# Optimization experiments

Measured on AMD Instinct MI355X. Metric: run time of the kernel, lower is better.

Reference implementation:

```python
import jax, jax.numpy as jnp
import numpy as np

EMBED_DIM = 1024
ZDIM = 128
STD = 0.02


def setup_inputs() -> dict:
    key = jax.random.key(0)
    ks = jax.random.split(key, 12)
    T, S, B, E, Z = 2048, 2048, 4, EMBED_DIM, ZDIM
    return {
        "query": jax.random.normal(ks[0], (T, B, E), jnp.float32),
        "key": jax.random.normal(ks[1], (S, B, E), jnp.float32),
        "Wq": jax.random.normal(ks[2], (2 * E + Z, E), jnp.float32) * STD,
        "bq": jnp.zeros((2 * E + Z,), jnp.float32),
        "Wk": jax.random.normal(ks[3], (Z, E), jnp.float32) * STD,
        "bk": jnp.zeros((Z,), jnp.float32),
        "Wv": jax.random.normal(ks[4], (E, E), jnp.float32) * STD,
        "bv": jnp.zeros((E,), jnp.float32),
        "Wh": jax.random.normal(ks[5], (E, E), jnp.float32) * STD,
        "bh": jnp.zeros((E,), jnp.float32),
        "gamma": jax.random.normal(ks[6], (2, Z), jnp.float32) * STD,
        "beta": jnp.zeros((2, Z), jnp.float32),
    }


def reference(query, key, Wq, bq, Wk, bk, Wv, bv, Wh, bh, gamma, beta):
    E, Z = EMBED_DIM, ZDIM
    scaling = Z ** (-0.5)
    # base: [T, B, 2E+Z]
    base = jnp.einsum('tbe,fe->tbf', query, Wq) + bq
    u = jax.nn.sigmoid(base[..., :E])                      # [T,B,E] output gate
    rq = jax.nn.silu(base[..., E:])                        # [T,B,E+Z]
    r = rq[..., :E]                                        # [T,B,E]
    q = rq[..., E:] * gamma[0] + beta[0]                   # [T,B,Z]
    k = jax.nn.silu(jnp.einsum('sbe,ze->sbz', key, Wk) + bk) * gamma[1] + beta[1]  # [S,B,Z]
    v = jax.nn.silu(jnp.einsum('sbe,fe->sbf', key, Wv) + bv)                       # [S,B,E]
    # softmax attention over context dim
    qk = jnp.einsum('tbz,sbz->bts', q * scaling, k)        # [B,T,S]
    attn = jax.nn.softmax(qk, axis=-1)
    h = jnp.einsum('bts,sbf->tbf', attn, v)                # [T,B,E]
    h = jnp.tanh(jnp.einsum('tbe,fe->tbf', h * r, Wh) + bh)
    out = query + u * (h - query)                          # addcmul
    return out
```

## Files before the change

### kernel.cpp

```cpp
#include <hip/hip_runtime.h>
#include <cstdint>
#include <cstddef>

using short8  = __attribute__((ext_vector_type(8))) short;
using floatx4 = __attribute__((ext_vector_type(4))) float;

#define DEV __device__ __forceinline__

DEV float u2f(unsigned short u){
  union { unsigned int i; float f; } c; c.i = ((unsigned int)u) << 16; return c.f;
}
DEV unsigned short f2u(float f){
  union { float f; unsigned int i; } c; c.f = f;
  unsigned int i = c.i;
  i += 0x7fffu + ((i >> 16) & 1u);
  return (unsigned short)(i >> 16);
}
DEV float sigmoidf_(float x){ return 1.0f / (1.0f + __expf(-x)); }
DEV float siluf_(float x){ return x / (1.0f + __expf(-x)); }

#define ASYNC_LD16(g, l) __builtin_amdgcn_global_load_lds( \
    (const __attribute__((address_space(1))) unsigned int*)(g), \
    (__attribute__((address_space(3))) unsigned int*)(l), 16, 0, 0)

#define MFMA_BF16 __builtin_amdgcn_mfma_f32_16x16x32_bf16

#define SBAR() asm volatile("s_barrier" ::: "memory")
#define LGKM0() asm volatile("s_waitcnt lgkmcnt(0)" ::: "memory")

constexpr float SCALING = 0.088388347648318447f;

__global__ __launch_bounds__(256) void cast_act(
    const float* __restrict__ q, const float* __restrict__ k,
    unsigned short* __restrict__ qo, unsigned short* __restrict__ ko)
{
  const int bid = blockIdx.x;
  const int e = threadIdx.x * 4;
  const float* src; unsigned short* dst;
  if (bid < 8192) {
    src = q + (long long)bid * 1024;
    dst = qo + (long long)bid * 1024;
  } else {
    const int m = bid - 8192;
    const int s = m >> 2, b = m & 3;
    src = k + (long long)m * 1024;
    dst = ko + ((long long)b * 2048 + s) * 1024;
  }
  const float4 v = *(const float4*)(src + e);
  ushort4 o; o.x=f2u(v.x); o.y=f2u(v.y); o.z=f2u(v.z); o.w=f2u(v.w);
  *(ushort4*)(dst + e) = o;
}

__global__ __launch_bounds__(256) void cast_w(
    const float* __restrict__ Wq, const float* __restrict__ Wk,
    const float* __restrict__ Wv, const float* __restrict__ Wh,
    unsigned short* __restrict__ oq, unsigned short* __restrict__ ok,
    unsigned short* __restrict__ ov, unsigned short* __restrict__ oh)
{
  const int bid = blockIdx.x;
  const int e = threadIdx.x * 4;
  const float* src; unsigned short* dst;
  if (bid < 2176)      { src = Wq + (long long)bid * 1024;        dst = oq + (long long)bid * 1024; }
  else if (bid < 2304) { src = Wk + (long long)(bid-2176) * 1024; dst = ok + (long long)(bid-2176) * 1024; }
  else if (bid < 3328) { src = Wv + (long long)(bid-2304) * 1024; dst = ov + (long long)(bid-2304) * 1024; }
  else                 { src = Wh + (long long)(bid-3328) * 1024; dst = oh + (long long)(bid-3328) * 1024; }
  const float4 v = *(const float4*)(src + e);
  ushort4 o; o.x=f2u(v.x); o.y=f2u(v.y); o.z=f2u(v.z); o.w=f2u(v.w);
  *(ushort4*)(dst + e) = o;
}

template<int EPI>
__global__ __launch_bounds__(256, 2)
void gemm_bt(const unsigned short* __restrict__ A, long long bsA, int lda,
             const unsigned short* __restrict__ Bm, long long bsB, int ldb,
             int K,
             float* __restrict__ f0,
             unsigned short* __restrict__ b0)
{
  __shared__ __align__(16) unsigned short As[128][64];
  __shared__ __align__(16) unsigned short Bs[128][64];

  const int tid = threadIdx.x;
  const int bm = blockIdx.x, bn = blockIdx.y, bz = blockIdx.z;
  const unsigned short* Ag = A  + (long long)bz * bsA;
  const unsigned short* Bg = Bm + (long long)bz * bsB;
  const int row0 = bm * 128;
  const int col0 = bn * 128;

  const int lane = tid & 63;
  const int wv   = tid >> 6;
  const int wm   = (wv & 1) * 64;
  const int wn   = (wv >> 1) * 64;
  const int lr   = lane & 15;
  const int lq   = lane >> 4;
  const int r7   = lr & 7;

  const unsigned short* gA[4]; const unsigned short* gB[4];
  unsigned short* lA[4]; unsigned short* lB[4];
  #pragma unroll
  for (int i = 0; i < 4; i++) {
    const int c  = tid + i * 256;
    const int rr = c >> 3;
    const int gc = (c & 7) ^ (rr & 7);
    gA[i] = Ag + (long long)(row0 + rr) * lda + gc * 8;
    gB[i] = Bg + (long long)(col0 + rr) * ldb + gc * 8;
    lA[i] = &As[0][0] + c * 8;
    lB[i] = &Bs[0][0] + c * 8;
  }

  floatx4 acc[4][4];
  const floatx4 zero = {0.f, 0.f, 0.f, 0.f};
  #pragma unroll
  for (int i = 0; i < 4; i++)
    #pragma unroll
    for (int j = 0; j < 4; j++) acc[i][j] = zero;

  for (int kt = 0; kt < K; kt += 64) {
    #pragma unroll
    for (int i = 0; i < 4; i++) {
      ASYNC_LD16(gA[i] + kt, lA[i]);
      ASYNC_LD16(gB[i] + kt, lB[i]);
    }
    __syncthreads();
    #pragma unroll
    for (int ks = 0; ks < 64; ks += 32) {
      const int k8 = ks >> 3;
      short8 af[4], bfv[4];
      #pragma unroll
      for (int i = 0; i < 4; i++) {
        const int sc = (lq + k8) ^ r7;
        af[i]  = *(const short8*)(&As[wm + i*16 + lr][sc * 8]);
        bfv[i] = *(const short8*)(&Bs[wn + i*16 + lr][sc * 8]);
      }
      #pragma unroll
      for (int mi = 0; mi < 4; mi++)
        #pragma unroll
        for (int ni = 0; ni < 4; ni++)
          acc[mi][ni] = MFMA_BF16(af[mi], bfv[ni], acc[mi][ni], 0, 0, 0);
    }
    __syncthreads();
  }

  #pragma unroll
  for (int mi = 0; mi < 4; mi++) {
    float s4[4];
    #pragma unroll
    for (int r = 0; r < 4; r++) s4[r] = 0.f;
    #pragma unroll
    for (int ni = 0; ni < 4; ni++) {
      #pragma unroll
      for (int r = 0; r < 4; r++) {
        const int gm = row0 + wm + mi * 16 + lq * 4 + r;
        const int gn = col0 + wn + ni * 16 + lr;
        const float e = __expf(acc[mi][ni][r] * SCALING);
        b0[(long long)bz * 2048 * 2048 + (long long)gm * 2048 + gn] = f2u(e);
        s4[r] += e;
      }
    }
    #pragma unroll
    for (int r = 0; r < 4; r++) {
      float s = s4[r];
      #pragma unroll
      for (int m2 = 8; m2 >= 1; m2 >>= 1) s += __shfl_xor(s, m2);
      if (lr == 0) {
        const int gm = row0 + wm + mi * 16 + lq * 4 + r;
        atomicAdd(f0 + (long long)bz * 2048 + gm, s);
      }
    }
  }
}

__global__ __launch_bounds__(256, 2)
void gemm_nz128(const unsigned short* __restrict__ A0, const unsigned short* __restrict__ A1,
                const unsigned short* __restrict__ B0, const unsigned short* __restrict__ B1,
                const float* __restrict__ bi0, const float* __restrict__ bi1,
                const float* __restrict__ g0,  const float* __restrict__ g1,
                const float* __restrict__ be0, const float* __restrict__ be1,
                unsigned short* __restrict__ o0, unsigned short* __restrict__ o1)
{
  __shared__ __align__(16) unsigned short As[128][64];
  __shared__ __align__(16) unsigned short Bs[128][64];

  const int tid = threadIdx.x;
  const int bm = blockIdx.x;
  const int z  = blockIdx.z;
  const unsigned short* Ag = z ? A1 : A0;
  const unsigned short* Bg = z ? B1 : B0;
  const float* bias = z ? bi1 : bi0;
  const float* gam  = z ? g1  : g0;
  const float* bet  = z ? be1 : be0;
  unsigned short* ob = z ? o1 : o0;
  const int row0 = bm * 128;

  const int lane = tid & 63;
  const int wv   = tid >> 6;
  const int wm   = (wv & 1) * 64;
  const int wn   = (wv >> 1) * 64;
  const int lr   = lane & 15;
  const int lq   = lane >> 4;
  const int r7   = lr & 7;

  const unsigned short* gA[4]; const unsigned short* gB[4];
  unsigned short* lA[4]; unsigned short* lB[4];
  #pragma unroll
  for (int i = 0; i < 4; i++) {
    const int c  = tid + i * 256;
    const int rr = c >> 3;
    const int gc = (c & 7) ^ (rr & 7);
    gA[i] = Ag + (long long)(row0 + rr) * 1024 + gc * 8;
    gB[i] = Bg + (long long)rr * 1024 + gc * 8;
    lA[i] = &As[0][0] + c * 8;
    lB[i] = &Bs[0][0] + c * 8;
  }

  floatx4 acc[4][4];
  const floatx4 zero = {0.f, 0.f, 0.f, 0.f};
  #pragma unroll
  for (int i = 0; i < 4; i++)
    #pragma unroll
    for (int j = 0; j < 4; j++) acc[i][j] = zero;

  for (int kt = 0; kt < 1024; kt += 64) {
    #pragma unroll
    for (int i = 0; i < 4; i++) {
      ASYNC_LD16(gA[i] + kt, lA[i]);
      ASYNC_LD16(gB[i] + kt, lB[i]);
    }
    __syncthreads();
    #pragma unroll
    for (int ks = 0; ks < 64; ks += 32) {
      const int k8 = ks >> 3;
      short8 af[4], bfv[4];
      #pragma unroll
      for (int i = 0; i < 4; i++) {
        const int sc = (lq + k8) ^ r7;
        af[i]  = *(const short8*)(&As[wm + i*16 + lr][sc * 8]);
        bfv[i] = *(const short8*)(&Bs[wn + i*16 + lr][sc * 8]);
      }
      #pragma unroll
      for (int mi = 0; mi < 4; mi++)
        #pragma unroll
        for (int ni = 0; ni < 4; ni++)
          acc[mi][ni] = MFMA_BF16(af[mi], bfv[ni], acc[mi][ni], 0, 0, 0);
    }
    __syncthreads();
  }

  #pragma unroll
  for (int mi = 0; mi < 4; mi++)
    #pragma unroll
    for (int ni = 0; ni < 4; ni++)
      #pragma unroll
      for (int r = 0; r < 4; r++) {
        const int gm = row0 + wm + mi * 16 + lq * 4 + r;
        const int gn = wn + ni * 16 + lr;
        float v = acc[mi][ni][r] + bias[gn];
        ob[(long long)gm * 128 + gn] = f2u(siluf_(v) * gam[gn] + bet[gn]);
      }
}

__global__ __launch_bounds__(512, 2)
void gemm256(const unsigned short* __restrict__ A, int lda,
             const unsigned short* __restrict__ Bm, int ldb,
             int K,
             const float* __restrict__ bias,
             float* __restrict__ f0,
             unsigned short* __restrict__ b0)
{
  __shared__ __align__(16) unsigned short Ls[65536];

  const int tid = threadIdx.x;
  const int bm = blockIdx.x, bn = blockIdx.y;
  const int row0 = bm * 256;
  const int col0 = bn * 256;

  const int lane = tid & 63;
  const int wv   = tid >> 6;
  const int wr   = (wv >> 2) * 128;
  const int wc   = (wv & 3) * 64;
  const int lr   = lane & 15;
  const int lq   = lane >> 4;
  const int r7   = lr & 7;

  const int rr0 = tid >> 3;
  const int swz = ((tid & 7) ^ (rr0 & 7)) * 8;
  const unsigned short* gA0 = A  + (long long)(row0 + rr0) * lda + swz;
  const unsigned short* gB0 = Bm + (long long)(col0 + rr0) * ldb + swz;
  const long long sA64 = 64LL * lda, sB64 = 64LL * ldb;
  unsigned short* lA0 = &Ls[0]     + tid * 8;
  unsigned short* lB0 = &Ls[16384] + tid * 8;

  floatx4 acc[8][4];
  const floatx4 zero = {0.f, 0.f, 0.f, 0.f};
  #pragma unroll
  for (int i = 0; i < 8; i++)
    #pragma unroll
    for (int j = 0; j < 4; j++) acc[i][j] = zero;

  const int NT = K >> 6;

  #pragma unroll
  for (int i = 0; i < 4; i++) ASYNC_LD16(gA0 + i * sA64,      lA0 + i * 4096);
  #pragma unroll
  for (int i = 0; i < 4; i++) ASYNC_LD16(gB0 + i * sB64,      lB0 + i * 4096);
  #pragma unroll
  for (int i = 0; i < 4; i++) ASYNC_LD16(gA0 + i * sA64 + 64, lA0 + i * 4096 + 32768);
  #pragma unroll
  for (int i = 0; i < 4; i++) ASYNC_LD16(gB0 + i * sB64 + 64, lB0 + i * 4096 + 32768);
  asm volatile("s_waitcnt vmcnt(8)" ::: "memory");
  SBAR();

  for (int t = 0; t < NT; ++t) {
    const int cb = (t & 1) << 15;
    const unsigned short* Ab = &Ls[cb];
    const unsigned short* Bb = &Ls[cb + 16384];
    const bool st = (t + 2) < NT;
    const int kt2 = (t + 2) << 6;

    short8 afA[4][2], afB[4][2], bf01[2][2], bf23[2][2];

    #pragma unroll
    for (int mi = 0; mi < 4; mi++)
      #pragma unroll
      for (int k = 0; k < 2; k++)
        afA[mi][k] = *(const short8*)(Ab + (wr + mi*16 + lr) * 64 + (((k<<2) + lq) ^ r7) * 8);
    #pragma unroll
    for (int ni = 0; ni < 2; ni++)
      #pragma unroll
      for (int k = 0; k < 2; k++)
        bf01[ni][k] = *(const short8*)(Bb + (wc + ni*16 + lr) * 64 + (((k<<2) + lq) ^ r7) * 8);
    #pragma unroll
    for (int ni = 0; ni < 2; ni++)
      #pragma unroll
      for (int k = 0; k < 2; k++)
        bf23[ni][k] = *(const short8*)(Bb + (wc + (ni+2)*16 + lr) * 64 + (((k<<2) + lq) ^ r7) * 8);
    __builtin_amdgcn_s_setprio(1);
    #pragma unroll
    for (int mi = 0; mi < 4; mi++)
      #pragma unroll
      for (int ni = 0; ni < 2; ni++)
        #pragma unroll
        for (int k = 0; k < 2; k++)
          acc[mi][ni] = MFMA_BF16(afA[mi][k], bf01[ni][k], acc[mi][ni], 0, 0, 0);
    #pragma unroll
    for (int mi = 0; mi < 4; mi++)
      #pragma unroll
      for (int ni = 0; ni < 2; ni++)
        #pragma unroll
        for (int k = 0; k < 2; k++)
          acc[mi][ni+2] = MFMA_BF16(afA[mi][k], bf23[ni][k], acc[mi][ni+2], 0, 0, 0);
    __builtin_amdgcn_s_setprio(0);
    LGKM0();
    SBAR();

    #pragma unroll
    for (int mi = 0; mi < 4; mi++)
      #pragma unroll
      for (int k = 0; k < 2; k++)
        afB[mi][k] = *(const short8*)(Ab + (wr + (mi+4)*16 + lr) * 64 + (((k<<2) + lq) ^ r7) * 8);
    if (st) {
      #pragma unroll
      for (int i = 0; i < 4; i++) ASYNC_LD16(gB0 + i * sB64 + kt2, lB0 + i * 4096 + cb);
    }
    __builtin_amdgcn_s_setprio(1);
    #pragma unroll
    for (int mi = 0; mi < 4; mi++)
      #pragma unroll
      for (int ni = 0; ni < 2; ni++)
        #pragma unroll
        for (int k = 0; k < 2; k++)
          acc[mi+4][ni] = MFMA_BF16(afB[mi][k], bf01[ni][k], acc[mi+4][ni], 0, 0, 0);
    __builtin_amdgcn_s_setprio(0);
    LGKM0();
    SBAR();

    if (st) {
      #pragma unroll
      for (int i = 0; i < 4; i++) ASYNC_LD16(gA0 + i * sA64 + kt2, lA0 + i * 4096 + cb);
    }
    __builtin_amdgcn_s_setprio(1);
    #pragma unroll
    for (int mi = 0; mi < 4; mi++)
      #pragma unroll
      for (int ni = 0; ni < 2; ni++)
        #pragma unroll
        for (int k = 0; k < 2; k++)
          acc[mi+4][ni+2] = MFMA_BF16(afB[mi][k], bf23[ni][k], acc[mi+4][ni+2], 0, 0, 0);
    __builtin_amdgcn_s_setprio(0);
    if (st) { asm volatile("s_waitcnt vmcnt(8)" ::: "memory"); }
    else    { asm volatile("s_waitcnt vmcnt(0)" ::: "memory"); }
    SBAR();
  }

  #pragma unroll
  for (int mi = 0; mi < 8; mi++)
    #pragma unroll
    for (int ni = 0; ni < 4; ni++)
      #pragma unroll
      for (int r = 0; r < 4; r++) {
        const int gm = row0 + wr + mi * 16 + lq * 4 + r;
        const int gn = col0 + wc + ni * 16 + lr;
        float v = acc[mi][ni][r] + bias[gn];
        if (gn < 1024) {
          ((unsigned short*)f0)[(long long)gm * 1024 + gn] = f2u(sigmoidf_(v));
        } else {
          b0[(long long)gm * 1024 + (gn - 1024)] = f2u(siluf_(v));
        }
      }
}

template<int EPI>
__global__ __launch_bounds__(512, 2)
void gemm_n128(const unsigned short* __restrict__ A, long long bsA, int lda,
               const unsigned short* __restrict__ Bm, long long bsB, int ldb,
               int K,
               const float* __restrict__ bias,
               float* __restrict__ f0,
               unsigned short* __restrict__ b0,
               const unsigned short* __restrict__ rmul,
               const float* __restrict__ qin)
{
  __shared__ __align__(16) unsigned short Ls[49152];

  const int tid = threadIdx.x;
  const int bm = blockIdx.x, bn = blockIdx.y, bz = blockIdx.z;
  const unsigned short* Ag = A  + (long long)bz * bsA;
  const unsigned short* Bg = Bm + (long long)bz * bsB;
  const int row0 = bm * 256;
  const int col0 = bn * 128;

  const int lane = tid & 63;
  const int wv   = tid >> 6;
  const int wr   = (wv & 3) * 64;
  const int wc   = (wv >> 2) * 64;
  const int lr   = lane & 15;
  const int lq   = lane >> 4;
  const int r7   = lr & 7;

  const int rr0 = tid >> 3;
  const int swz = ((tid & 7) ^ (rr0 & 7)) * 8;
  const unsigned short* gA0 = Ag + (long long)(row0 + rr0) * lda + swz;
  const unsigned short* gB0 = Bg + (long long)(col0 + rr0) * ldb + swz;
  const long long sA64 = 64LL * lda, sB64 = 64LL * ldb;
  unsigned short* lA0 = &Ls[0]     + tid * 8;
  unsigned short* lB0 = &Ls[16384] + tid * 8;

  floatx4 acc[4][4];
  const floatx4 zero = {0.f, 0.f, 0.f, 0.f};
  #pragma unroll
  for (int i = 0; i < 4; i++)
    #pragma unroll
    for (int j = 0; j < 4; j++) acc[i][j] = zero;

  const int NT = K >> 6;

  #pragma unroll
  for (int i = 0; i < 4; i++) ASYNC_LD16(gA0 + i * sA64,      lA0 + i * 4096);
  #pragma unroll
  for (int i = 0; i < 2; i++) ASYNC_LD16(gB0 + i * sB64,      lB0 + i * 4096);
  #pragma unroll
  for (int i = 0; i < 4; i++) ASYNC_LD16(gA0 + i * sA64 + 64, lA0 + i * 4096 + 24576);
  #pragma unroll
  for (int i = 0; i < 2; i++) ASYNC_LD16(gB0 + i * sB64 + 64, lB0 + i * 4096 + 24576);
  asm volatile("s_waitcnt vmcnt(6)" ::: "memory");
  SBAR();

  for (int t = 0; t < NT; ++t) {
    const int cb = (t & 1) * 24576;
    const unsigned short* Ab = &Ls[cb];
    const unsigned short* Bb = &Ls[cb + 16384];
    const bool st = (t + 2) < NT;
    const int kt2 = (t + 2) << 6;

    short8 afA[4][2], bfv[4][2];

    #pragma unroll
    for (int mi = 0; mi < 4; mi++)
      #pragma unroll
      for (int k = 0; k < 2; k++)
        afA[mi][k] = *(const short8*)(Ab + (wr + mi*16 + lr) * 64 + (((k<<2) + lq) ^ r7) * 8);
    #pragma unroll
    for (int ni = 0; ni < 4; ni++)
      #pragma unroll
      for (int k = 0; k < 2; k++)
        bfv[ni][k] = *(const short8*)(Bb + (wc + ni*16 + lr) * 64 + (((k<<2) + lq) ^ r7) * 8);
    __builtin_amdgcn_s_setprio(1);
    #pragma unroll
    for (int mi = 0; mi < 4; mi++)
      #pragma unroll
      for (int ni = 0; ni < 2; ni++)
        #pragma unroll
        for (int k = 0; k < 2; k++)
          acc[mi][ni] = MFMA_BF16(afA[mi][k], bfv[ni][k], acc[mi][ni], 0, 0, 0);
    __builtin_amdgcn_s_setprio(0);
    LGKM0();
    SBAR();

    if (st) {
      #pragma unroll
      for (int i = 0; i < 4; i++) ASYNC_LD16(gA0 + i * sA64 + kt2, lA0 + i * 4096 + cb);
      #pragma unroll
      for (int i = 0; i < 2; i++) ASYNC_LD16(gB0 + i * sB64 + kt2, lB0 + i * 4096 + cb);
    }
    __builtin_amdgcn_s_setprio(1);
    #pragma unroll
    for (int mi = 0; mi < 4; mi++)
      #pragma unroll
      for (int ni = 0; ni < 2; ni++)
        #pragma unroll
        for (int k = 0; k < 2; k++)
          acc[mi][ni+2] = MFMA_BF16(afA[mi][k], bfv[ni+2][k], acc[mi][ni+2], 0, 0, 0);
    __builtin_amdgcn_s_setprio(0);
    if (st) { asm volatile("s_waitcnt vmcnt(6)" ::: "memory"); }
    else    { asm volatile("s_waitcnt vmcnt(0)" ::: "memory"); }
    SBAR();
  }

  #pragma unroll
  for (int mi = 0; mi < 4; mi++) {
    float iv[4];
    if constexpr (EPI == 4) {
      #pragma unroll
      for (int r = 0; r < 4; r++) {
        const int gm = row0 + wr + mi * 16 + lq * 4 + r;
        iv[r] = 1.0f / f0[(long long)bz * 2048 + gm];
      }
    }
    #pragma unroll
    for (int ni = 0; ni < 4; ni++) {
      #pragma unroll
      for (int r = 0; r < 4; r++) {
        const int gm = row0 + wr + mi * 16 + lq * 4 + r;
        const int gn = col0 + wc + ni * 16 + lr;
        float v = acc[mi][ni][r];
        if constexpr (EPI == 2) {
          v += bias[gm];
          const int b = gn >> 11, s = gn & 2047;
          b0[((long long)b * 1024 + gm) * 2048 + s] = f2u(siluf_(v));
        } else if constexpr (EPI == 4) {
          const long long idx = ((long long)gm * 4 + bz) * 1024 + gn;
          b0[idx] = f2u(v * iv[r] * u2f(rmul[idx]));
        } else {
          const long long idx = (long long)gm * 1024 + gn;
          const float tv = tanhf(v + bias[gn]);
          const float qv = qin[idx];
          f0[idx] = qv + u2f(rmul[idx]) * (tv - qv);
        }
      }
    }
  }
}

extern "C" void kernel_launch(void* const* d_in, const int* in_sizes, int n_in,
                              void* d_out, int out_size, void* d_ws, size_t ws_size,
                              hipStream_t stream)
{
  (void)in_sizes; (void)n_in; (void)out_size; (void)ws_size;
  const float* query = (const float*)d_in[0];
  const float* key   = (const float*)d_in[1];
  const float* Wq    = (const float*)d_in[2];
  const float* bq    = (const float*)d_in[3];
  const float* Wk    = (const float*)d_in[4];
  const float* bk    = (const float*)d_in[5];
  const float* Wv    = (const float*)d_in[6];
  const float* bv    = (const float*)d_in[7];
  const float* Wh    = (const float*)d_in[8];
  const float* bh    = (const float*)d_in[9];
  const float* gamma = (const float*)d_in[10];
  const float* beta  = (const float*)d_in[11];
  float* out = (float*)d_out;

  char* p = (char*)d_ws;
  auto take = [&](size_t bytes) -> char* {
    char* r = p; p += (bytes + 255) & ~(size_t)255; return r;
  };
  unsigned short* qbf = (unsigned short*)take(8192ULL * 1024 * 2);
  unsigned short* kbr = (unsigned short*)take(8192ULL * 1024 * 2);
  unsigned short* Wqb = (unsigned short*)take(2176ULL * 1024 * 2);
  unsigned short* Wkb = (unsigned short*)take(128ULL  * 1024 * 2);
  unsigned short* Wvb = (unsigned short*)take(1024ULL * 1024 * 2);
  unsigned short* Whb = (unsigned short*)take(1024ULL * 1024 * 2);
  unsigned short* ub  = (unsigned short*)take(8192ULL * 1024 * 2);
  unsigned short* rbf = (unsigned short*)take(8192ULL * 1024 * 2);
  unsigned short* qpj = (unsigned short*)take(8192ULL * 128 * 2);
  unsigned short* kpj = (unsigned short*)take(8192ULL * 128 * 2);
  unsigned short* vT  = (unsigned short*)take(4ULL * 1024 * 2048 * 2);
  unsigned short* Pb  = (unsigned short*)take(4ULL * 2048 * 2048 * 2);
  unsigned short* hrb = (unsigned short*)take(8192ULL * 1024 * 2);
  float*          rs  = (float*)take(4ULL * 2048 * 4);

  dim3 blk(256);
  dim3 gblk(512);
  cast_act<<<16384, blk, 0, stream>>>(query, key, qbf, kbr);
  cast_w<<<4352, blk, 0, stream>>>(Wq, Wk, Wv, Wh, Wqb, Wkb, Wvb, Whb);
  hipMemsetAsync(rs, 0, 4ULL * 2048 * 4, stream);

  gemm_nz128<<<dim3(64, 1, 2), blk, 0, stream>>>(
      qbf, kbr, Wqb + 2048LL * 1024, Wkb,
      bq + 2048, bk, gamma, gamma + 128, beta, beta + 128, qpj, kpj);
  gemm256<<<dim3(32, 8, 1), gblk, 0, stream>>>(qbf, 1024, Wqb, 1024, 1024,
      bq, (float*)ub, rbf);
  gemm_n128<2><<<dim3(4, 64, 1), gblk, 0, stream>>>(Wvb, 0, 1024, kbr, 0, 1024, 1024,
      bv, nullptr, vT, nullptr, nullptr);
  gemm_bt<3><<<dim3(16, 16, 4), blk, 0, stream>>>(qpj, 128, 512, kpj, 2048LL * 128, 128, 128,
      rs, Pb);
  gemm_n128<4><<<dim3(8, 8, 4), gblk, 0, stream>>>(Pb, 2048LL * 2048, 2048,
      vT, 1024LL * 2048, 2048, 2048,
      nullptr, rs, hrb, rbf, nullptr);
  gemm_n128<5><<<dim3(32, 8, 1), gblk, 0, stream>>>(hrb, 0, 1024, Whb, 0, 1024, 1024,
      bh, out, nullptr, ub, query);
}
```

Before: 347.7 us.

## Fuse QK^T exp and PV matmul into one flash-style attention kernel

Replaces the separate score kernel, which wrote the full bf16 probability matrix plus atomic row sums, and the P·V GEMM with one fused kernel. Each block computes a 64-row tile of exp scores per 64-key chunk into shared memory, multiplies it against a V tile, and gets the row sums by an MFMA against a ones vector. The intent is to remove the 32 MB P round trip through global memory, the memset and the atomics. In exchange, each block of 64 rows by 512 output columns recomputes QK^T twice (once per E-half), and the max subtraction is skipped as before. It also moves the LGKM wait ahead of the MFMAs in the generic GEMM, with a sched barrier.

```diff
diff --git a/kernel.cpp b/kernel.cpp
--- a/kernel.cpp
+++ b/kernel.cpp
@@ -69,107 +69,6 @@
   *(ushort4*)(dst + e) = o;
 }
 
-template<int EPI>
-__global__ __launch_bounds__(256, 2)
-void gemm_bt(const unsigned short* __restrict__ A, long long bsA, int lda,
-             const unsigned short* __restrict__ Bm, long long bsB, int ldb,
-             int K,
-             float* __restrict__ f0,
-             unsigned short* __restrict__ b0)
-{
-  __shared__ __align__(16) unsigned short As[128][64];
-  __shared__ __align__(16) unsigned short Bs[128][64];
-
-  const int tid = threadIdx.x;
-  const int bm = blockIdx.x, bn = blockIdx.y, bz = blockIdx.z;
-  const unsigned short* Ag = A  + (long long)bz * bsA;
-  const unsigned short* Bg = Bm + (long long)bz * bsB;
-  const int row0 = bm * 128;
-  const int col0 = bn * 128;
-
-  const int lane = tid & 63;
-  const int wv   = tid >> 6;
-  const int wm   = (wv & 1) * 64;
-  const int wn   = (wv >> 1) * 64;
-  const int lr   = lane & 15;
-  const int lq   = lane >> 4;
-  const int r7   = lr & 7;
-
-  const unsigned short* gA[4]; const unsigned short* gB[4];
-  unsigned short* lA[4]; unsigned short* lB[4];
-  #pragma unroll
-  for (int i = 0; i < 4; i++) {
-    const int c  = tid + i * 256;
-    const int rr = c >> 3;
-    const int gc = (c & 7) ^ (rr & 7);
-    gA[i] = Ag + (long long)(row0 + rr) * lda + gc * 8;
-    gB[i] = Bg + (long long)(col0 + rr) * ldb + gc * 8;
-    lA[i] = &As[0][0] + c * 8;
-    lB[i] = &Bs[0][0] + c * 8;
-  }
-
-  floatx4 acc[4][4];
-  const floatx4 zero = {0.f, 0.f, 0.f, 0.f};
-  #pragma unroll
-  for (int i = 0; i < 4; i++)
-    #pragma unroll
-    for (int j = 0; j < 4; j++) acc[i][j] = zero;
-
-  for (int kt = 0; kt < K; kt += 64) {
-    #pragma unroll
-    for (int i = 0; i < 4; i++) {
-      ASYNC_LD16(gA[i] + kt, lA[i]);
-      ASYNC_LD16(gB[i] + kt, lB[i]);
-    }
-    __syncthreads();
-    #pragma unroll
-    for (int ks = 0; ks < 64; ks += 32) {
-      const int k8 = ks >> 3;
-      short8 af[4], bfv[4];
-      #pragma unroll
-      for (int i = 0; i < 4; i++) {
-        const int sc = (lq + k8) ^ r7;
-        af[i]  = *(const short8*)(&As[wm + i*16 + lr][sc * 8]);
-        bfv[i] = *(const short8*)(&Bs[wn + i*16 + lr][sc * 8]);
-      }
-      #pragma unroll
-      for (int mi = 0; mi < 4; mi++)
-        #pragma unroll
-        for (int ni = 0; ni < 4; ni++)
-          acc[mi][ni] = MFMA_BF16(af[mi], bfv[ni], acc[mi][ni], 0, 0, 0);
-    }
-    __syncthreads();
-  }
-
-  #pragma unroll
-  for (int mi = 0; mi < 4; mi++) {
-    float s4[4];
-    #pragma unroll
-    for (int r = 0; r < 4; r++) s4[r] = 0.f;
-    #pragma unroll
-    for (int ni = 0; ni < 4; ni++) {
-      #pragma unroll
-      for (int r = 0; r < 4; r++) {
-        const int gm = row0 + wm + mi * 16 + lq * 4 + r;
-        const int gn = col0 + wn + ni * 16 + lr;
-        const float e = __expf(acc[mi][ni][r] * SCALING);
-        b0[(long long)bz * 2048 * 2048 + (long long)gm * 2048 + gn] = f2u(e);
-        s4[r] += e;
-      }
-    }
-    #pragma unroll
-    for (int r = 0; r < 4; r++) {
-      float s = s4[r];
-      #pragma unroll
-      for (int m2 = 8; m2 >= 1; m2 >>= 1) s += __shfl_xor(s, m2);
-      if (lr == 0) {
-        const int gm = row0 + wm + mi * 16 + lq * 4 + r;
-        atomicAdd(f0 + (long long)bz * 2048 + gm, s);
-      }
-    }
-  }
-}
-
 __global__ __launch_bounds__(256, 2)
 void gemm_nz128(const unsigned short* __restrict__ A0, const unsigned short* __restrict__ A1,
                 const unsigned short* __restrict__ B0, const unsigned short* __restrict__ B1,
@@ -484,6 +383,8 @@
       #pragma unroll
       for (int k = 0; k < 2; k++)
         bfv[ni][k] = *(const short8*)(Bb + (wc + ni*16 + lr) * 64 + (((k<<2) + lq) ^ r7) * 8);
+    LGKM0();
+    __builtin_amdgcn_sched_barrier(0);
     __builtin_amdgcn_s_setprio(1);
     #pragma unroll
     for (int mi = 0; mi < 4; mi++)
@@ -493,7 +394,6 @@
         for (int k = 0; k < 2; k++)
           acc[mi][ni] = MFMA_BF16(afA[mi][k], bfv[ni][k], acc[mi][ni], 0, 0, 0);
     __builtin_amdgcn_s_setprio(0);
-    LGKM0();
     SBAR();
 
     if (st) {
@@ -518,14 +418,6 @@
 
   #pragma unroll
   for (int mi = 0; mi < 4; mi++) {
-    float iv[4];
-    if constexpr (EPI == 4) {
-      #pragma unroll
-      for (int r = 0; r < 4; r++) {
-        const int gm = row0 + wr + mi * 16 + lq * 4 + r;
-        iv[r] = 1.0f / f0[(long long)bz * 2048 + gm];
-      }
-    }
     #pragma unroll
     for (int ni = 0; ni < 4; ni++) {
       #pragma unroll
@@ -537,15 +429,178 @@
           v += bias[gm];
           const int b = gn >> 11, s = gn & 2047;
           b0[((long long)b * 1024 + gm) * 2048 + s] = f2u(siluf_(v));
-        } else if constexpr (EPI == 4) {
-          const long long idx = ((long long)gm * 4 + bz) * 1024 + gn;
-          b0[idx] = f2u(v * iv[r] * u2f(rmul[idx]));
         } else {
           const long long idx = (long long)gm * 1024 + gn;
           const float tv = tanhf(v + bias[gn]);
           const float qv = qin[idx];
           f0[idx] = qv + u2f(rmul[idx]) * (tv - qv);
         }
+      }
+    }
+  }
+}
+
+__global__ __launch_bounds__(512, 2)
+void attn_fused(const unsigned short* __restrict__ qpj,
+                const unsigned short* __restrict__ kpj,
+                const unsigned short* __restrict__ vT,
+                const unsigned short* __restrict__ rbf,
+                unsigned short* __restrict__ hrb)
+{
+  __shared__ __align__(16) unsigned short Vs[32768];
+  __shared__ __align__(16) unsigned short Ks[2][8192];
+  __shared__ __align__(16) unsigned short Ps[4096];
+  __shared__ float rsl[64];
+
+  const int tid = threadIdx.x;
+  const int eh = blockIdx.x, ty = blockIdx.y, bz = blockIdx.z;
+  const int t0 = ty * 64;
+
+  const int lane = tid & 63;
+  const int wv   = tid >> 6;
+  const int lr   = lane & 15;
+  const int lq   = lane >> 4;
+  const int mi_s = wv & 3;
+  const int niA  = (wv >> 2) * 2;
+
+  const unsigned short* kb_g = kpj + (long long)bz * 2048 * 128;
+  const unsigned short* vb_g = vT  + (long long)bz * 1024 * 2048;
+
+  short8 afq[4];
+  {
+    const unsigned short* qrow = qpj + (long long)bz * 128
+                               + (long long)(t0 + mi_s * 16 + lr) * 512;
+    #pragma unroll
+    for (int kd = 0; kd < 4; kd++)
+      afq[kd] = *(const short8*)(qrow + (kd * 4 + lq) * 8);
+  }
+
+  const int rrV = tid >> 3;
+  const int gcV = ((tid & 7) ^ (rrV & 7)) * 8;
+  const unsigned short* gV0 = vb_g + (long long)(eh * 512 + rrV) * 2048 + gcV;
+  unsigned short* lV0 = Vs + tid * 8;
+  const int rrK = tid >> 4;
+  const int gcK = ((tid & 15) ^ (rrK & 15)) * 8;
+  const unsigned short* gK0 = kb_g + (long long)rrK * 128 + gcK;
+  unsigned short* lK0 = &Ks[0][0] + tid * 8;
+
+  floatx4 acc[4][4];
+  floatx4 accSum[4];
+  const floatx4 zero = {0.f, 0.f, 0.f, 0.f};
+  #pragma unroll
+  for (int i = 0; i < 4; i++) {
+    accSum[i] = zero;
+    #pragma unroll
+    for (int j = 0; j < 4; j++) acc[i][j] = zero;
+  }
+  const short ob = (short)0x3F80;
+  const short8 ones = {ob, ob, ob, ob, ob, ob, ob, ob};
+
+  #pragma unroll
+  for (int i = 0; i < 2; i++) ASYNC_LD16(gK0 + i * 4096, lK0 + i * 4096);
+
+  for (int t = 0; t < 32; ++t) {
+    const unsigned short* Kb = &Ks[t & 1][0];
+    const bool st = (t + 1) < 32;
+
+    #pragma unroll
+    for (int i = 0; i < 8; i++)
+      ASYNC_LD16(gV0 + (long long)i * 131072 + t * 64, lV0 + i * 4096);
+    if (st) {
+      unsigned short* lKn = &Ks[(t + 1) & 1][0] + tid * 8;
+      #pragma unroll
+      for (int i = 0; i < 2; i++)
+        ASYNC_LD16(gK0 + (long long)(t + 1) * 8192 + i * 4096, lKn + i * 4096);
+    }
+    if (st) { asm volatile("s_waitcnt vmcnt(10)" ::: "memory"); }
+    else    { asm volatile("s_waitcnt vmcnt(8)"  ::: "memory"); }
+    SBAR();
+
+    floatx4 accS[2] = {zero, zero};
+    short8 bfk[2][4];
+    #pragma unroll
+    for (int f = 0; f < 2; f++)
+      #pragma unroll
+      for (int kd = 0; kd < 4; kd++)
+        bfk[f][kd] = *(const short8*)(Kb + ((niA + f) * 16 + lr) * 128
+                                         + (((kd * 4 + lq) ^ lr) & 15) * 8);
+    #pragma unroll
+    for (int f = 0; f < 2; f++)
+      #pragma unroll
+      for (int kd = 0; kd < 4; kd++)
+        accS[f] = MFMA_BF16(afq[kd], bfk[f][kd], accS[f], 0, 0, 0);
+    #pragma unroll
+    for (int f = 0; f < 2; f++) {
+      const int nif = niA + f;
+      #pragma unroll
+      for (int r = 0; r < 4; r++) {
+        const float e = __expf(accS[f][r] * SCALING);
+        const int trow = mi_s * 16 + lq * 4 + r;
+        const int scol = nif * 16 + lr;
+        const int slot = (scol >> 3) ^ (trow & 7);
+        Ps[trow * 64 + slot * 8 + (lr & 7)] = f2u(e);
+      }
+    }
+    LGKM0();
+    if (st) { asm volatile("s_waitcnt vmcnt(2)" ::: "memory"); }
+    else    { asm volatile("s_waitcnt vmcnt(0)" ::: "memory"); }
+    SBAR();
+
+    short8 afP[4][2], bfv[4][2];
+    #pragma unroll
+    for (int mi = 0; mi < 4; mi++)
+      #pragma unroll
+      for (int k8 = 0; k8 < 2; k8++)
+        afP[mi][k8] = *(const short8*)(Ps + (mi * 16 + lr) * 64
+                                          + ((k8 * 4 + lq) ^ (lr & 7)) * 8);
+    #pragma unroll
+    for (int ni = 0; ni < 4; ni++)
+      #pragma unroll
+      for (int k8 = 0; k8 < 2; k8++)
+        bfv[ni][k8] = *(const short8*)(Vs + (wv * 64 + ni * 16 + lr) * 64
+                                          + ((k8 * 4 + lq) ^ (lr & 7)) * 8);
+    __builtin_amdgcn_s_setprio(1);
+    #pragma unroll
+    for (int mi = 0; mi < 4; mi++)
+      #pragma unroll
+      for (int ni = 0; ni < 4; ni++)
+        #pragma unroll
+        for (int k8 = 0; k8 < 2; k8++)
+          acc[mi][ni] = MFMA_BF16(afP[mi][k8], bfv[ni][k8], acc[mi][ni], 0, 0, 0);
+    __builtin_amdgcn_s_setprio(0);
+    if (wv == 0) {
+      #pragma unroll
+      for (int mi = 0; mi < 4; mi++)
+        #pragma unroll
+        for (int k8 = 0; k8 < 2; k8++)
+          accSum[mi] = MFMA_BF16(afP[mi][k8], ones, accSum[mi], 0, 0, 0);
+    }
+    LGKM0();
+    SBAR();
+  }
+
+  if (wv == 0 && lr == 0) {
+    #pragma unroll
+    for (int mi = 0; mi < 4; mi++)
+      #pragma unroll
+      for (int r = 0; r < 4; r++)
+        rsl[mi * 16 + lq * 4 + r] = accSum[mi][r];
+  }
+  LGKM0();
+  SBAR();
+  #pragma unroll
+  for (int mi = 0; mi < 4; mi++) {
+    float iv[4];
+    #pragma unroll
+    for (int r = 0; r < 4; r++) iv[r] = 1.0f / rsl[mi * 16 + lq * 4 + r];
+    #pragma unroll
+    for (int ni = 0; ni < 4; ni++) {
+      #pragma unroll
+      for (int r = 0; r < 4; r++) {
+        const int gt = t0 + mi * 16 + lq * 4 + r;
+        const int ge = eh * 512 + wv * 64 + ni * 16 + lr;
+        const long long idx = ((long long)gt * 4 + bz) * 1024 + ge;
+        hrb[idx] = f2u(acc[mi][ni][r] * iv[r] * u2f(rbf[idx]));
       }
     }
   }
@@ -585,15 +640,12 @@
   unsigned short* qpj = (unsigned short*)take(8192ULL * 128 * 2);
   unsigned short* kpj = (unsigned short*)take(8192ULL * 128 * 2);
   unsigned short* vT  = (unsigned short*)take(4ULL * 1024 * 2048 * 2);
-  unsigned short* Pb  = (unsigned short*)take(4ULL * 2048 * 2048 * 2);
   unsigned short* hrb = (unsigned short*)take(8192ULL * 1024 * 2);
-  float*          rs  = (float*)take(4ULL * 2048 * 4);
 
   dim3 blk(256);
   dim3 gblk(512);
   cast_act<<<16384, blk, 0, stream>>>(query, key, qbf, kbr);
   cast_w<<<4352, blk, 0, stream>>>(Wq, Wk, Wv, Wh, Wqb, Wkb, Wvb, Whb);
-  hipMemsetAsync(rs, 0, 4ULL * 2048 * 4, stream);
 
   gemm_nz128<<<dim3(64, 1, 2), blk, 0, stream>>>(
       qbf, kbr, Wqb + 2048LL * 1024, Wkb,
@@ -602,11 +654,7 @@
       bq, (float*)ub, rbf);
   gemm_n128<2><<<dim3(4, 64, 1), gblk, 0, stream>>>(Wvb, 0, 1024, kbr, 0, 1024, 1024,
       bv, nullptr, vT, nullptr, nullptr);
-  gemm_bt<3><<<dim3(16, 16, 4), blk, 0, stream>>>(qpj, 128, 512, kpj, 2048LL * 128, 128, 128,
-      rs, Pb);
-  gemm_n128<4><<<dim3(8, 8, 4), gblk, 0, stream>>>(Pb, 2048LL * 2048, 2048,
-      vT, 1024LL * 2048, 2048, 2048,
-      nullptr, rs, hrb, rbf, nullptr);
+  attn_fused<<<dim3(2, 32, 4), gblk, 0, stream>>>(qpj, kpj, vT, rbf, hrb);
   gemm_n128<5><<<dim3(32, 8, 1), gblk, 0, stream>>>(hrb, 0, 1024, Whb, 0, 1024, 1024,
       bh, out, nullptr, ub, query);
 }
```

Result: no change. 341.0 us (-1.9%).
